# Performance work log

Measured on AMD Instinct MI355X. Metric: run time of the kernel, lower is better.

The kernel has to match this reference:

```python
import jax, jax.numpy as jnp
import numpy as np


def setup_inputs() -> dict:
    key = jax.random.key(0)
    k0, k1, k2 = jax.random.split(key, 3)
    B, S, H, D = 2, 2048, 16, 128  # flash-attn layout [batch, seq, heads, head_dim]
    q = jax.random.normal(k0, (B, S, H, D), dtype=jnp.float32)
    k = jax.random.normal(k1, (B, S, H, D), dtype=jnp.float32)
    v = jax.random.normal(k2, (B, S, H, D), dtype=jnp.float32)
    return {"_in0": q, "_in1": k, "_in2": v}


def reference(_in0, _in1, _in2):
    # Ring attention computes exact (non-causal, default) scaled dot-product
    # attention over the full sequence; the ring KV rotation is a distributed
    # execution detail, not a change in math. Single-device math:
    q, k, v = _in0, _in1, _in2
    D = q.shape[-1]
    scale = 1.0 / jnp.sqrt(jnp.asarray(D, dtype=q.dtype))
    # scores: [B, H, Sq, Sk]
    scores = jnp.einsum("bqhd,bkhd->bhqk", q, k) * scale
    probs = jax.nn.softmax(scores, axis=-1)
    out = jnp.einsum("bhqk,bkhd->bqhd", probs, v)
    return out
```

## Files before the change

### kernel.cpp

```cpp
#include <hip/hip_runtime.h>
#include <hip/hip_bf16.h>

typedef __attribute__((ext_vector_type(8))) short short8;
typedef __attribute__((ext_vector_type(16))) float f32x16;
typedef __attribute__((ext_vector_type(4))) unsigned int uint4v;

#define NB 2
#define NS 2048
#define NH 16
#define ND 128
#define ROWS (NH * ND)
#define KVBLK 64
#define QBLK 256
#define NTILE (NS / KVBLK)
#define NQB (NS / QBLK)
#define NWIN (NTILE / 2)
#define TILEB 16384

__device__ __forceinline__ unsigned short f2bf(float f) {
  union { __hip_bfloat16 b; unsigned short u; } c;
  c.b = __float2bfloat16(f);
  return c.u;
}

__device__ __forceinline__ short8 pack8(float4 a, float4 b, float s) {
  short8 r;
  r[0] = (short)f2bf(a.x * s); r[1] = (short)f2bf(a.y * s);
  r[2] = (short)f2bf(a.z * s); r[3] = (short)f2bf(a.w * s);
  r[4] = (short)f2bf(b.x * s); r[5] = (short)f2bf(b.y * s);
  r[6] = (short)f2bf(b.z * s); r[7] = (short)f2bf(b.w * s);
  return r;
}

__device__ __forceinline__ void dma16(const void* g, void* l) {
  __builtin_amdgcn_global_load_lds(
      (const __attribute__((address_space(1))) unsigned int*)g,
      (__attribute__((address_space(3))) unsigned int*)l, 16, 0, 0);
}

__device__ __forceinline__ void pl32swap(unsigned int& a, unsigned int& b) {
  asm("v_permlane32_swap_b32 %0, %1" : "+v"(a), "+v"(b));
}

__global__ __launch_bounds__(256) void prepass_kv(
    const float* __restrict__ Kg, const float* __restrict__ Vg,
    char* __restrict__ Kbt, char* __restrict__ Vbt) {
  const int blk = blockIdx.x;
  const int t = blk & (NTILE - 1);
  const int bh = blk >> 5;
  const int h = bh & (NH - 1);
  const int b = bh >> 4;
  const int tid = threadIdx.x;

  const size_t ibase = (size_t)b * NS * ROWS + (size_t)h * ND + (size_t)t * KVBLK * ROWS;
  const float* Kp = Kg + ibase;
  const float* Vp = Vg + ibase;
  char* Kt = Kbt + (size_t)blk * TILEB;
  char* Vt = Vbt + (size_t)blk * TILEB;

#pragma unroll
  for (int j = 0; j < 4; ++j) {
    const int r = j * 16 + (tid >> 4);
    const int c = tid & 15;
    const float* src = Kp + (size_t)r * ROWS + c * 8;
    float4 a = *reinterpret_cast<const float4*>(src);
    float4 d = *reinterpret_cast<const float4*>(src + 4);
    *reinterpret_cast<short8*>(Kt + r * 256 + (((c ^ (r & 15)) << 4))) = pack8(a, d, 1.0f);
  }

  __shared__ float vt[64][129];
#pragma unroll
  for (int j = 0; j < 4; ++j) {
    const int r = j * 16 + (tid >> 4);
    const int c0 = (tid & 15) * 8;
    float4 a = *reinterpret_cast<const float4*>(Vp + (size_t)r * ROWS + c0);
    float4 d = *reinterpret_cast<const float4*>(Vp + (size_t)r * ROWS + c0 + 4);
    vt[r][c0 + 0] = a.x; vt[r][c0 + 1] = a.y; vt[r][c0 + 2] = a.z; vt[r][c0 + 3] = a.w;
    vt[r][c0 + 4] = d.x; vt[r][c0 + 5] = d.y; vt[r][c0 + 6] = d.z; vt[r][c0 + 7] = d.w;
  }
  __syncthreads();
#pragma unroll
  for (int it = 0; it < 4; ++it) {
    const int item = it * 256 + tid;
    const int r = item >> 4;
    const int j = item & 15;
    const int d = 2 * r + (j >> 3);
    const int k0 = (j & 7) * 8;
    short8 o8;
#pragma unroll
    for (int i = 0; i < 8; ++i) o8[i] = (short)f2bf(vt[k0 + i][d]);
    *reinterpret_cast<short8*>(Vt + r * 256 + (((j ^ (r & 15)) << 4))) = o8;
  }
}

__global__ __launch_bounds__(512, 2) void fattn_fwd(
    const float* __restrict__ Qg, const char* __restrict__ Kbt,
    const char* __restrict__ Vbt, float* __restrict__ Og) {
  __shared__ __align__(16) char lds[131072];
  const int tid = threadIdx.x;
  const int l = tid & 63;
  const int w = tid >> 6;
  const int l31 = l & 31;
  const int hi2 = l >> 5;

  const int orig = blockIdx.x;
  const int wg = (orig & 7) * 32 + (orig >> 3);
  const int qblk = wg & (NQB - 1);
  const int bh = wg >> 3;
  const int h = bh & (NH - 1);
  const int b = bh >> 4;

  const float* Qp = Qg + (size_t)b * NS * ROWS + (size_t)h * ND;
  float* Op = Og + (size_t)b * NS * ROWS + (size_t)h * ND;
  const char* Ktiles = Kbt + (size_t)bh * NTILE * TILEB;
  const char* Vtiles = Vbt + (size_t)bh * NTILE * TILEB;

  const float scale = 0.08838834764831845f * 1.4426950408889634f;

  const int qrow = qblk * QBLK + w * 32 + l31;
  short8 qf[8];
  {
    const float* qr = Qp + (size_t)qrow * ROWS + hi2 * 8;
#pragma unroll
    for (int ks = 0; ks < 8; ++ks) {
      float4 a = *reinterpret_cast<const float4*>(qr + ks * 16);
      float4 c = *reinterpret_cast<const float4*>(qr + ks * 16 + 4);
      qf[ks] = pack8(a, c, scale);
    }
  }

  int qkoff[8], pvoff[4];
  {
    const int rsw = (l31 & 15) << 4;
#pragma unroll
    for (int ks = 0; ks < 8; ++ks)
      qkoff[ks] = l31 * 256 + ((ks * 32 + hi2 * 16) ^ rsw);
    const int vsw = ((l31 >> 1) & 15) << 4;
#pragma unroll
    for (int ks = 0; ks < 4; ++ks)
      pvoff[ks] = (l31 >> 1) * 256 +
                  ((((l31 & 1) * 128) + ks * 32 + hi2 * 16) ^ vsw);
  }

  auto stageT = [&](int t, int s) {
    const char* Ks = Ktiles + (size_t)t * TILEB;
    const char* Vs = Vtiles + (size_t)t * TILEB;
    char* kd = lds + s * 32768;
    char* vd = kd + 16384;
#pragma unroll
    for (int i = 0; i < 2; ++i) {
      const int off = i * 8192 + w * 1024;
      dma16(Ks + off + l * 16, kd + off);
      dma16(Vs + off + l * 16, vd + off);
    }
  };

  f32x16 o[4];
#pragma unroll
  for (int dt = 0; dt < 4; ++dt) o[dt] = 0.f;
  float l_acc = 0.f;

  auto qkc = [&](const char* kb) -> f32x16 {
    f32x16 a = 0.f;
#pragma unroll
    for (int ks = 0; ks < 8; ++ks) {
      short8 kf = *reinterpret_cast<const short8*>(kb + qkoff[ks]);
      a = __builtin_amdgcn_mfma_f32_32x32x16_bf16(kf, qf[ks], a, 0, 0, 0);
    }
    return a;
  };

  auto sm = [&](const f32x16& acc, short8& f0, short8& f1) {
    f32x16 p;
#pragma unroll
    for (int r = 0; r < 16; ++r) p[r] = exp2f(acc[r]);
    float s01 = (p[0] + p[1]) + (p[2] + p[3]);
    float s23 = (p[4] + p[5]) + (p[6] + p[7]);
    float s45 = (p[8] + p[9]) + (p[10] + p[11]);
    float s67 = (p[12] + p[13]) + (p[14] + p[15]);
    l_acc += (s01 + s23) + (s45 + s67);
    unsigned int X[4];
#pragma unroll
    for (int j = 0; j < 4; ++j)
      X[j] = (unsigned int)f2bf(p[2 * j]) | ((unsigned int)f2bf(p[2 * j + 1]) << 16);
    pl32swap(X[0], X[2]);
    pl32swap(X[1], X[3]);
    uint4v u0 = {X[0], X[1], X[2], X[3]};
    f0 = __builtin_bit_cast(short8, u0);
    unsigned int Y[4];
#pragma unroll
    for (int j = 0; j < 4; ++j)
      Y[j] = (unsigned int)f2bf(p[8 + 2 * j]) | ((unsigned int)f2bf(p[8 + 2 * j + 1]) << 16);
    pl32swap(Y[0], Y[2]);
    pl32swap(Y[1], Y[3]);
    uint4v u1 = {Y[0], Y[1], Y[2], Y[3]};
    f1 = __builtin_bit_cast(short8, u1);
  };

  auto pvh = [&](const char* vb, int ks0, short8 f0, short8 f1) {
#pragma unroll
    for (int dt = 0; dt < 4; ++dt) {
      short8 v0 = *reinterpret_cast<const short8*>(vb + pvoff[ks0] + dt * 4096);
      o[dt] = __builtin_amdgcn_mfma_f32_32x32x16_bf16(v0, f0, o[dt], 0, 0, 0);
      short8 v1 = *reinterpret_cast<const short8*>(vb + pvoff[ks0 + 1] + dt * 4096);
      o[dt] = __builtin_amdgcn_mfma_f32_32x32x16_bf16(v1, f1, o[dt], 0, 0, 0);
    }
  };

  stageT(0, 0);
  stageT(1, 1);
  asm volatile("s_waitcnt vmcnt(0)" ::: "memory");
  __syncthreads();

#pragma unroll 1
  for (int j = 0; j < NWIN; ++j) {
    if (j + 1 < NWIN) {
      const int s0 = ((j & 1) ^ 1) * 2;
      stageT(2 * j + 2, s0);
      stageT(2 * j + 3, s0 + 1);
    }
    const char* kb0 = lds + (j & 1) * 65536;
    const char* kb1 = kb0 + 32768;
    const char* vb0 = kb0 + 16384;
    const char* vb1 = kb1 + 16384;

    f32x16 a0 = qkc(kb0);
    f32x16 a1 = qkc(kb0 + 8192);
    f32x16 a2 = qkc(kb1);
    f32x16 a3 = qkc(kb1 + 8192);
    short8 p00, p01, p10, p11;
    sm(a0, p00, p01);
    sm(a1, p10, p11);
    pvh(vb0, 0, p00, p01);
    pvh(vb0, 2, p10, p11);
    short8 p20, p21, p30, p31;
    sm(a2, p20, p21);
    sm(a3, p30, p31);
    pvh(vb1, 0, p20, p21);
    pvh(vb1, 2, p30, p31);

    if (j + 1 < NWIN) {
      asm volatile("s_waitcnt vmcnt(0)" ::: "memory");
      __syncthreads();
    }
  }

  const float lt = l_acc + __shfl_xor(l_acc, 32);
  const float inv = 1.0f / lt;
  float* orow = Op + (size_t)qrow * ROWS;
#pragma unroll
  for (int dt = 0; dt < 4; ++dt) {
#pragma unroll
    for (int g = 0; g < 4; ++g) {
      float4 v;
      v.x = o[dt][g * 4 + 0] * inv;
      v.y = o[dt][g * 4 + 1] * inv;
      v.z = o[dt][g * 4 + 2] * inv;
      v.w = o[dt][g * 4 + 3] * inv;
      *reinterpret_cast<float4*>(orow + dt * 32 + g * 8 + hi2 * 4) = v;
    }
  }
}

extern "C" void kernel_launch(void* const* d_in, const int* in_sizes, int n_in,
                              void* d_out, int out_size, void* d_ws, size_t ws_size,
                              hipStream_t stream) {
  const float* q = (const float*)d_in[0];
  const float* k = (const float*)d_in[1];
  const float* v = (const float*)d_in[2];
  float* out = (float*)d_out;
  (void)in_sizes; (void)n_in; (void)out_size; (void)ws_size;
  char* Kbt = (char*)d_ws;
  char* Vbt = Kbt + (size_t)NB * NH * NTILE * TILEB;
  prepass_kv<<<dim3(NB * NH * NTILE), dim3(256), 0, stream>>>(k, v, Kbt, Vbt);
  fattn_fwd<<<dim3(NQB * NB * NH), dim3(512), 0, stream>>>(q, Kbt, Vbt, out);
}
```

Baseline: 108.2 us.

## Pre-arrange K/V tiles in MFMA fragment order and use native exp2

The prepass now writes K and V tiles in the exact per-lane MFMA operand order, so each fragment sits at a contiguous 16-byte slot indexed by lane. The attention kernel no longer needs the swizzled per-lane offset arrays, which frees registers and simplifies LDS address math to lane*16 plus constants. The prepass now also stages K through LDS, which adds a sync and shared-memory traffic there. exp2f is replaced with the raw hardware exp2 builtin, which skips range handling and risks slight precision differences for extreme inputs.

```diff
diff --git a/kernel.cpp b/kernel.cpp
--- a/kernel.cpp
+++ b/kernel.cpp
@@ -42,9 +42,13 @@
   asm("v_permlane32_swap_b32 %0, %1" : "+v"(a), "+v"(b));
 }
 
+__device__ __forceinline__ float fexp2(float x) {
+  return __builtin_amdgcn_exp2f(x);
+}
+
 __global__ __launch_bounds__(256) void prepass_kv(
     const float* __restrict__ Kg, const float* __restrict__ Vg,
-    char* __restrict__ Kbt, char* __restrict__ Vbt) {
+    char* __restrict__ Kimg, char* __restrict__ Vimg) {
   const int blk = blockIdx.x;
   const int t = blk & (NTILE - 1);
   const int bh = blk >> 5;
@@ -55,53 +59,69 @@
   const size_t ibase = (size_t)b * NS * ROWS + (size_t)h * ND + (size_t)t * KVBLK * ROWS;
   const float* Kp = Kg + ibase;
   const float* Vp = Vg + ibase;
-  char* Kt = Kbt + (size_t)blk * TILEB;
-  char* Vt = Vbt + (size_t)blk * TILEB;
+  char* Kt = Kimg + (size_t)blk * TILEB;
+  char* Vt = Vimg + (size_t)blk * TILEB;
+
+  __shared__ float st[64][129];
 
 #pragma unroll
   for (int j = 0; j < 4; ++j) {
     const int r = j * 16 + (tid >> 4);
-    const int c = tid & 15;
-    const float* src = Kp + (size_t)r * ROWS + c * 8;
-    float4 a = *reinterpret_cast<const float4*>(src);
-    float4 d = *reinterpret_cast<const float4*>(src + 4);
-    *reinterpret_cast<short8*>(Kt + r * 256 + (((c ^ (r & 15)) << 4))) = pack8(a, d, 1.0f);
-  }
-
-  __shared__ float vt[64][129];
+    const int c0 = (tid & 15) * 8;
+    float4 a = *reinterpret_cast<const float4*>(Kp + (size_t)r * ROWS + c0);
+    float4 d = *reinterpret_cast<const float4*>(Kp + (size_t)r * ROWS + c0 + 4);
+    st[r][c0 + 0] = a.x; st[r][c0 + 1] = a.y; st[r][c0 + 2] = a.z; st[r][c0 + 3] = a.w;
+    st[r][c0 + 4] = d.x; st[r][c0 + 5] = d.y; st[r][c0 + 6] = d.z; st[r][c0 + 7] = d.w;
+  }
+  __syncthreads();
+#pragma unroll
+  for (int it = 0; it < 4; ++it) {
+    const int item = it * 256 + tid;
+    const int g = item >> 6;
+    const int ll = item & 63;
+    const int row = (g >> 3) * 32 + (ll & 31);
+    const int kc = (g & 7) * 16 + (ll >> 5) * 8;
+    short8 o8;
+#pragma unroll
+    for (int e = 0; e < 8; ++e) o8[e] = (short)f2bf(st[row][kc + e]);
+    *reinterpret_cast<short8*>(Kt + (g * 64 + ll) * 16) = o8;
+  }
+  __syncthreads();
+
 #pragma unroll
   for (int j = 0; j < 4; ++j) {
     const int r = j * 16 + (tid >> 4);
     const int c0 = (tid & 15) * 8;
     float4 a = *reinterpret_cast<const float4*>(Vp + (size_t)r * ROWS + c0);
     float4 d = *reinterpret_cast<const float4*>(Vp + (size_t)r * ROWS + c0 + 4);
-    vt[r][c0 + 0] = a.x; vt[r][c0 + 1] = a.y; vt[r][c0 + 2] = a.z; vt[r][c0 + 3] = a.w;
-    vt[r][c0 + 4] = d.x; vt[r][c0 + 5] = d.y; vt[r][c0 + 6] = d.z; vt[r][c0 + 7] = d.w;
+    st[r][c0 + 0] = a.x; st[r][c0 + 1] = a.y; st[r][c0 + 2] = a.z; st[r][c0 + 3] = a.w;
+    st[r][c0 + 4] = d.x; st[r][c0 + 5] = d.y; st[r][c0 + 6] = d.z; st[r][c0 + 7] = d.w;
   }
   __syncthreads();
 #pragma unroll
   for (int it = 0; it < 4; ++it) {
     const int item = it * 256 + tid;
-    const int r = item >> 4;
-    const int j = item & 15;
-    const int d = 2 * r + (j >> 3);
-    const int k0 = (j & 7) * 8;
+    const int g = item >> 6;
+    const int ll = item & 63;
+    const int d = (g >> 2) * 32 + (ll & 31);
+    const int kv = (g & 3) * 16 + (ll >> 5) * 8;
     short8 o8;
 #pragma unroll
-    for (int i = 0; i < 8; ++i) o8[i] = (short)f2bf(vt[k0 + i][d]);
-    *reinterpret_cast<short8*>(Vt + r * 256 + (((j ^ (r & 15)) << 4))) = o8;
+    for (int e = 0; e < 8; ++e) o8[e] = (short)f2bf(st[kv + e][d]);
+    *reinterpret_cast<short8*>(Vt + (g * 64 + ll) * 16) = o8;
   }
 }
 
 __global__ __launch_bounds__(512, 2) void fattn_fwd(
-    const float* __restrict__ Qg, const char* __restrict__ Kbt,
-    const char* __restrict__ Vbt, float* __restrict__ Og) {
+    const float* __restrict__ Qg, const char* __restrict__ Kimg,
+    const char* __restrict__ Vimg, float* __restrict__ Og) {
   __shared__ __align__(16) char lds[131072];
   const int tid = threadIdx.x;
   const int l = tid & 63;
   const int w = tid >> 6;
   const int l31 = l & 31;
   const int hi2 = l >> 5;
+  const int lo16 = l * 16;
 
   const int orig = blockIdx.x;
   const int wg = (orig & 7) * 32 + (orig >> 3);
@@ -112,8 +132,8 @@
 
   const float* Qp = Qg + (size_t)b * NS * ROWS + (size_t)h * ND;
   float* Op = Og + (size_t)b * NS * ROWS + (size_t)h * ND;
-  const char* Ktiles = Kbt + (size_t)bh * NTILE * TILEB;
-  const char* Vtiles = Vbt + (size_t)bh * NTILE * TILEB;
+  const char* Ktiles = Kimg + (size_t)bh * NTILE * TILEB;
+  const char* Vtiles = Vimg + (size_t)bh * NTILE * TILEB;
 
   const float scale = 0.08838834764831845f * 1.4426950408889634f;
 
@@ -127,19 +147,6 @@
       float4 c = *reinterpret_cast<const float4*>(qr + ks * 16 + 4);
       qf[ks] = pack8(a, c, scale);
     }
-  }
-
-  int qkoff[8], pvoff[4];
-  {
-    const int rsw = (l31 & 15) << 4;
-#pragma unroll
-    for (int ks = 0; ks < 8; ++ks)
-      qkoff[ks] = l31 * 256 + ((ks * 32 + hi2 * 16) ^ rsw);
-    const int vsw = ((l31 >> 1) & 15) << 4;
-#pragma unroll
-    for (int ks = 0; ks < 4; ++ks)
-      pvoff[ks] = (l31 >> 1) * 256 +
-                  ((((l31 & 1) * 128) + ks * 32 + hi2 * 16) ^ vsw);
   }
 
   auto stageT = [&](int t, int s) {
@@ -150,8 +157,8 @@
 #pragma unroll
     for (int i = 0; i < 2; ++i) {
       const int off = i * 8192 + w * 1024;
-      dma16(Ks + off + l * 16, kd + off);
-      dma16(Vs + off + l * 16, vd + off);
+      dma16(Ks + off + lo16, kd + off);
+      dma16(Vs + off + lo16, vd + off);
     }
   };
 
@@ -160,11 +167,11 @@
   for (int dt = 0; dt < 4; ++dt) o[dt] = 0.f;
   float l_acc = 0.f;
 
-  auto qkc = [&](const char* kb) -> f32x16 {
+  auto qkc = [&](const char* kb, int mtbase) -> f32x16 {
     f32x16 a = 0.f;
 #pragma unroll
     for (int ks = 0; ks < 8; ++ks) {
-      short8 kf = *reinterpret_cast<const short8*>(kb + qkoff[ks]);
+      short8 kf = *reinterpret_cast<const short8*>(kb + lo16 + (mtbase + ks) * 1024);
       a = __builtin_amdgcn_mfma_f32_32x32x16_bf16(kf, qf[ks], a, 0, 0, 0);
     }
     return a;
@@ -173,7 +180,7 @@
   auto sm = [&](const f32x16& acc, short8& f0, short8& f1) {
     f32x16 p;
 #pragma unroll
-    for (int r = 0; r < 16; ++r) p[r] = exp2f(acc[r]);
+    for (int r = 0; r < 16; ++r) p[r] = fexp2(acc[r]);
     float s01 = (p[0] + p[1]) + (p[2] + p[3]);
     float s23 = (p[4] + p[5]) + (p[6] + p[7]);
     float s45 = (p[8] + p[9]) + (p[10] + p[11]);
@@ -200,9 +207,9 @@
   auto pvh = [&](const char* vb, int ks0, short8 f0, short8 f1) {
 #pragma unroll
     for (int dt = 0; dt < 4; ++dt) {
-      short8 v0 = *reinterpret_cast<const short8*>(vb + pvoff[ks0] + dt * 4096);
+      short8 v0 = *reinterpret_cast<const short8*>(vb + lo16 + (dt * 4 + ks0) * 1024);
       o[dt] = __builtin_amdgcn_mfma_f32_32x32x16_bf16(v0, f0, o[dt], 0, 0, 0);
-      short8 v1 = *reinterpret_cast<const short8*>(vb + pvoff[ks0 + 1] + dt * 4096);
+      short8 v1 = *reinterpret_cast<const short8*>(vb + lo16 + (dt * 4 + ks0 + 1) * 1024);
       o[dt] = __builtin_amdgcn_mfma_f32_32x32x16_bf16(v1, f1, o[dt], 0, 0, 0);
     }
   };
@@ -224,10 +231,10 @@
     const char* vb0 = kb0 + 16384;
     const char* vb1 = kb1 + 16384;
 
-    f32x16 a0 = qkc(kb0);
-    f32x16 a1 = qkc(kb0 + 8192);
-    f32x16 a2 = qkc(kb1);
-    f32x16 a3 = qkc(kb1 + 8192);
+    f32x16 a0 = qkc(kb0, 0);
+    f32x16 a1 = qkc(kb0, 8);
+    f32x16 a2 = qkc(kb1, 0);
+    f32x16 a3 = qkc(kb1, 8);
     short8 p00, p01, p10, p11;
     sm(a0, p00, p01);
     sm(a1, p10, p11);
@@ -270,8 +277,8 @@
   const float* v = (const float*)d_in[2];
   float* out = (float*)d_out;
   (void)in_sizes; (void)n_in; (void)out_size; (void)ws_size;
-  char* Kbt = (char*)d_ws;
-  char* Vbt = Kbt + (size_t)NB * NH * NTILE * TILEB;
-  prepass_kv<<<dim3(NB * NH * NTILE), dim3(256), 0, stream>>>(k, v, Kbt, Vbt);
-  fattn_fwd<<<dim3(NQB * NB * NH), dim3(512), 0, stream>>>(q, Kbt, Vbt, out);
-}
+  char* Kimg = (char*)d_ws;
+  char* Vimg = Kimg + (size_t)NB * NH * NTILE * TILEB;
+  prepass_kv<<<dim3(NB * NH * NTILE), dim3(256), 0, stream>>>(k, v, Kimg, Vimg);
+  fattn_fwd<<<dim3(NQB * NB * NH), dim3(512), 0, stream>>>(q, Kimg, Vimg, out);
+}
```

Result: faster. 97.43 us (median of 2 runs) (-10.0%).
